# Performance work log

Measured on AMD Instinct MI355X. Metric: run time of the kernel, lower is better.

## Reference

```python
import jax, jax.numpy as jnp
import numpy as np

C = 256
DK = C // 8  # query/key channels


def setup_inputs() -> dict:
    key = jax.random.key(0)
    ks = jax.random.split(key, 7)
    B, W, H = 4, 64, 64
    x = jax.random.normal(ks[0], (B, C, W, H), dtype=jnp.float32)
    s_in = 1.0 / np.sqrt(C)
    Wq = jax.random.normal(ks[1], (DK, C), dtype=jnp.float32) * s_in
    bq = jnp.zeros((DK,), dtype=jnp.float32)
    Wk = jax.random.normal(ks[2], (DK, C), dtype=jnp.float32) * s_in
    bk = jnp.zeros((DK,), dtype=jnp.float32)
    Wv = jax.random.normal(ks[3], (C, C), dtype=jnp.float32) * s_in
    bv = jnp.zeros((C,), dtype=jnp.float32)
    return {"x": x, "Wq": Wq, "bq": bq, "Wk": Wk, "bk": bk, "Wv": Wv, "bv": bv}


def reference(x, Wq, bq, Wk, bk, Wv, bv):
    B, Cc, W, H = x.shape
    N = W * H
    xf = x.reshape(B, Cc, N)  # (B, C, N) flattened spatial
    # 1x1 convs == channel matmuls
    q = jnp.einsum('dc,bcn->bnd', Wq, xf) + bq  # (B, N, DK)
    k = jnp.einsum('dc,bcn->bdn', Wk, xf) + bk[None, :, None]  # (B, DK, N)
    v = jnp.einsum('oc,bcn->bon', Wv, xf) + bv[None, :, None]  # (B, C, N)
    energy = jnp.einsum('bnd,bdm->bnm', q, k) / jnp.sqrt(jnp.float32(q.shape[-1]))
    attn = jax.nn.softmax(energy, axis=-1)  # (B, N, N)
    out = jnp.einsum('bcn,bmn->bcm', v, attn)  # v @ attn^T
    return out.reshape(B, Cc, W, H) + x
```

## Files before the change

kernel.cpp:

```cpp
#include <hip/hip_runtime.h>
#include <hip/hip_bf16.h>
#include <math.h>

#define BB 4
#define CC 256
#define DKK 32
#define NN 4096
#define QSCALE 0.17677669529663687f

typedef __attribute__((ext_vector_type(8))) __bf16 bf16x8;
typedef __attribute__((ext_vector_type(4))) __bf16 bf16x4;
typedef __attribute__((ext_vector_type(4))) float f32x4;

__global__ __launch_bounds__(256) void prep_kernel(
    const float* __restrict__ x, __bf16* __restrict__ xT,
    const float* __restrict__ Wq, const float* __restrict__ Wk,
    const float* __restrict__ Wv, __bf16* __restrict__ Wb)
{
    __shared__ float xs[64][68];
    const int tid = threadIdx.x;
    const int n0 = blockIdx.x * 64;
    const int c0 = blockIdx.y * 64;
    const int b  = blockIdx.z;

    if (b == 0) {
        int unit = blockIdx.y * 64 + blockIdx.x;
        if (unit < 80) {
            int i = (unit * 256 + tid) * 4;
            int row = i >> 8, col = i & 255;
            const float* src;
            if (row < 32)      src = &Wq[row * 256 + col];
            else if (row < 64) src = &Wk[(row - 32) * 256 + col];
            else               src = &Wv[(row - 64) * 256 + col];
            float4 v = *(const float4*)src;
            Wb[i]     = (__bf16)v.x;
            Wb[i + 1] = (__bf16)v.y;
            Wb[i + 2] = (__bf16)v.z;
            Wb[i + 3] = (__bf16)v.w;
        }
    }

#pragma unroll
    for (int p = 0; p < 4; p++) {
        int cc = p * 16 + (tid >> 4);
        int nf = (tid & 15) * 4;
        float4 v = *(const float4*)&x[((size_t)(b * CC + c0 + cc)) * NN + n0 + nf];
        xs[cc][nf] = v.x; xs[cc][nf + 1] = v.y; xs[cc][nf + 2] = v.z; xs[cc][nf + 3] = v.w;
    }
    __syncthreads();
    int n = tid >> 2, cs = (tid & 3) * 16;
    bf16x8 lo, hi;
#pragma unroll
    for (int j = 0; j < 8; j++) {
        lo[j] = (__bf16)xs[cs + j][n];
        hi[j] = (__bf16)xs[cs + 8 + j][n];
    }
    size_t base = ((size_t)(b * NN + n0 + n)) * CC + c0 + cs;
    *(bf16x8*)&xT[base]     = lo;
    *(bf16x8*)&xT[base + 8] = hi;
}

__global__ __launch_bounds__(256) void qkv_kernel(
    const __bf16* __restrict__ xT, const __bf16* __restrict__ Wb,
    const float* __restrict__ bq, const float* __restrict__ bk,
    const float* __restrict__ bv,
    __bf16* __restrict__ qws, __bf16* __restrict__ kws, __bf16* __restrict__ vws)
{
    __shared__ float scr[64][33];

    const int tid = threadIdx.x;
    const int w   = tid >> 6;
    const int l   = tid & 63;
    const int l15 = l & 15;
    const int lq  = l >> 4;
    const int n0  = blockIdx.x * 32;
    const int b   = blockIdx.y;

    const __bf16* xbase = xT + ((size_t)b * NN + n0 + l15) * CC + lq * 8;
    const __bf16* wbase = Wb + (size_t)(80 * w + l15) * CC + lq * 8;

    const f32x4 zf = {0.f, 0.f, 0.f, 0.f};
    f32x4 acc[5][2];
#pragma unroll
    for (int i = 0; i < 5; i++)
#pragma unroll
        for (int j = 0; j < 2; j++) acc[i][j] = zf;

    bf16x8 bcur[2], acur[5], bnxt[2], anxt[5];
#pragma unroll
    for (int nt = 0; nt < 2; nt++) bcur[nt] = *(const bf16x8*)(xbase + nt * 16 * CC);
#pragma unroll
    for (int ot = 0; ot < 5; ot++) acur[ot] = *(const bf16x8*)(wbase + ot * 16 * CC);

#pragma unroll
    for (int ks = 0; ks < 8; ks++) {
        if (ks < 7) {
#pragma unroll
            for (int nt = 0; nt < 2; nt++)
                bnxt[nt] = *(const bf16x8*)(xbase + nt * 16 * CC + (ks + 1) * 32);
#pragma unroll
            for (int ot = 0; ot < 5; ot++)
                anxt[ot] = *(const bf16x8*)(wbase + ot * 16 * CC + (ks + 1) * 32);
        }
#pragma unroll
        for (int ot = 0; ot < 5; ot++)
#pragma unroll
            for (int nt = 0; nt < 2; nt++)
                acc[ot][nt] = __builtin_amdgcn_mfma_f32_16x16x32_bf16(acur[ot], bcur[nt], acc[ot][nt], 0, 0, 0);
        if (ks < 7) {
#pragma unroll
            for (int nt = 0; nt < 2; nt++) bcur[nt] = bnxt[nt];
#pragma unroll
            for (int ot = 0; ot < 5; ot++) acur[ot] = anxt[ot];
        }
    }

    __bf16* vchunk = vws + (size_t)b * CC * NN + (size_t)(n0 >> 5) * 16 * 512;
#pragma unroll
    for (int ot = 0; ot < 5; ot++) {
        int ob = 80 * w + ot * 16;
#pragma unroll
        for (int nt = 0; nt < 2; nt++) {
#pragma unroll
            for (int r = 0; r < 4; r++) {
                int o = ob + lq * 4 + r;
                int n = nt * 16 + l15;
                float val = acc[ot][nt][r];
                if (ob >= 64) {
                    int c = o - 64;
                    vchunk[(5 * w - 4 + ot) * 512 + (lq * 4 + r) * 32 + n] =
                        (__bf16)(val + bv[c]);
                } else if (ob < 32) {
                    scr[o][n] = (val + bq[o]) * QSCALE;
                } else {
                    scr[o][n] = val + bk[o - 32];
                }
            }
        }
    }
    __syncthreads();
    {
        int n  = tid >> 3;
        int d0 = (tid & 7) * 4;
        bf16x4 qv, kv;
#pragma unroll
        for (int j = 0; j < 4; j++) {
            qv[j] = (__bf16)scr[d0 + j][n];
            kv[j] = (__bf16)scr[32 + d0 + j][n];
        }
        size_t base = ((size_t)b * NN + n0 + n) * DKK + d0;
        *(bf16x4*)&qws[base] = qv;
        *(bf16x4*)&kws[base] = kv;
    }
}

#define PST 40
#define MST 68
#define PWSZ (64 * PST)

__global__ __launch_bounds__(256, 2) void attn_kernel(
    const __bf16* __restrict__ qb, const __bf16* __restrict__ kb,
    const __bf16* __restrict__ vt, const float* __restrict__ x,
    float* __restrict__ out)
{
    __shared__ __align__(16) unsigned char smem[42240];
    __bf16* pw   = (__bf16*)smem + (threadIdx.x >> 6) * 2 * PWSZ;
    float*  Ls   = (float*)(smem + 40960);
    float*  Linv = (float*)(smem + 41984);

    const int tid = threadIdx.x;
    const int w   = tid >> 6;
    const int l   = tid & 63;
    const int l15 = l & 15;
    const int lq  = l >> 4;

    const int beta = blockIdx.x;
    const int b    = (beta >> 1) & 3;
    const int ch   = (beta >> 3) & 1;
    const int mt   = ((beta >> 4) << 1) | (beta & 1);
    const int m0   = mt * 64;

    const __bf16* qbb = qb + (size_t)b * NN * DKK;
    const __bf16* kbb = kb + (size_t)b * NN * DKK;
    const __bf16* vtb = vt + (size_t)b * CC * NN;

    bf16x8 qa[4];
#pragma unroll
    for (int af = 0; af < 4; af++)
        qa[af] = *(const bf16x8*)(qbb + (size_t)(m0 + af * 16 + l15) * DKK + lq * 8);

    const __bf16* kstrip = kbb + (size_t)(w * 32 + l15) * DKK + lq * 8;
    const __bf16* vstrip = vtb + (size_t)w * 8192 + (size_t)ch * 4096
                               + l15 * 32 + lq * 8;

    const f32x4 zf = {0.f, 0.f, 0.f, 0.f};
    f32x4 acc[4][8];
#pragma unroll
    for (int i = 0; i < 4; i++)
#pragma unroll
        for (int j = 0; j < 8; j++) acc[i][j] = zf;
    float lacc[4] = {0.f, 0.f, 0.f, 0.f};

    bf16x8 kA0 = *(const bf16x8*)kstrip;
    bf16x8 kA1 = *(const bf16x8*)(kstrip + 16 * DKK);
#pragma unroll
    for (int af = 0; af < 4; af++) {
        f32x4 e0 = __builtin_amdgcn_mfma_f32_16x16x32_bf16(kA0, qa[af], zf, 0, 0, 0);
        f32x4 e1 = __builtin_amdgcn_mfma_f32_16x16x32_bf16(kA1, qa[af], zf, 0, 0, 0);
        bf16x4 p0, p1;
#pragma unroll
        for (int r = 0; r < 4; r++) {
            float v0 = __expf(e0[r]); lacc[af] += v0; p0[r] = (__bf16)v0;
            float v1 = __expf(e1[r]); lacc[af] += v1; p1[r] = (__bf16)v1;
        }
        *(bf16x4*)&pw[(af * 16 + l15) * PST + lq * 4]      = p0;
        *(bf16x4*)&pw[(af * 16 + l15) * PST + 16 + lq * 4] = p1;
    }
    kA0 = *(const bf16x8*)(kstrip + (size_t)128 * DKK);
    kA1 = *(const bf16x8*)(kstrip + (size_t)144 * DKK);

#pragma unroll 2
    for (int ic = 0; ic < 31; ic++) {
        const int cur = ic & 1;
        const __bf16* vch = vstrip + (size_t)ic * 32768;

        bf16x8 vfC[4], vfN[4];
#pragma unroll
        for (int ct = 0; ct < 4; ct++)
            vfC[ct] = *(const bf16x8*)(vch + ct * 512);

        bf16x8 pf[4];
#pragma unroll
        for (int af = 0; af < 4; af++)
            pf[af] = *(const bf16x8*)&pw[cur * PWSZ + (af * 16 + l15) * PST + lq * 8];

#pragma unroll
        for (int af = 0; af < 4; af++) {
            f32x4 e0 = __builtin_amdgcn_mfma_f32_16x16x32_bf16(kA0, qa[af], zf, 0, 0, 0);
            f32x4 e1 = __builtin_amdgcn_mfma_f32_16x16x32_bf16(kA1, qa[af], zf, 0, 0, 0);
            bf16x4 p0, p1;
#pragma unroll
            for (int r = 0; r < 4; r++) {
                float v0 = __expf(e0[r]); lacc[af] += v0; p0[r] = (__bf16)v0;
                float v1 = __expf(e1[r]); lacc[af] += v1; p1[r] = (__bf16)v1;
            }
            *(bf16x4*)&pw[(cur ^ 1) * PWSZ + (af * 16 + l15) * PST + lq * 4]      = p0;
            *(bf16x4*)&pw[(cur ^ 1) * PWSZ + (af * 16 + l15) * PST + 16 + lq * 4] = p1;
        }
        kA0 = *(const bf16x8*)(kstrip + (size_t)(ic + 2) * 128 * DKK);
        kA1 = *(const bf16x8*)(kstrip + (size_t)((ic + 2) * 128 + 16) * DKK);

#pragma unroll
        for (int ct = 0; ct < 4; ct++)
            vfN[ct] = *(const bf16x8*)(vch + (4 + ct) * 512);
#pragma unroll
        for (int ct = 0; ct < 4; ct++)
#pragma unroll
            for (int af = 0; af < 4; af++)
                acc[af][ct] = __builtin_amdgcn_mfma_f32_16x16x32_bf16(vfC[ct], pf[af], acc[af][ct], 0, 0, 0);
#pragma unroll
        for (int ct = 0; ct < 4; ct++)
#pragma unroll
            for (int af = 0; af < 4; af++)
                acc[af][4 + ct] = __builtin_amdgcn_mfma_f32_16x16x32_bf16(vfN[ct], pf[af], acc[af][4 + ct], 0, 0, 0);
    }

    {
        const __bf16* vch = vstrip + (size_t)31 * 32768;
        bf16x8 pf[4];
#pragma unroll
        for (int af = 0; af < 4; af++)
            pf[af] = *(const bf16x8*)&pw[(31 & 1) * PWSZ + (af * 16 + l15) * PST + lq * 8];
        bf16x8 vfC[4], vfN[4];
#pragma unroll
        for (int ct = 0; ct < 4; ct++) vfC[ct] = *(const bf16x8*)(vch + ct * 512);
#pragma unroll
        for (int ct = 0; ct < 4; ct++) vfN[ct] = *(const bf16x8*)(vch + (4 + ct) * 512);
#pragma unroll
        for (int ct = 0; ct < 4; ct++)
#pragma unroll
            for (int af = 0; af < 4; af++)
                acc[af][ct] = __builtin_amdgcn_mfma_f32_16x16x32_bf16(vfC[ct], pf[af], acc[af][ct], 0, 0, 0);
#pragma unroll
        for (int ct = 0; ct < 4; ct++)
#pragma unroll
            for (int af = 0; af < 4; af++)
                acc[af][4 + ct] = __builtin_amdgcn_mfma_f32_16x16x32_bf16(vfN[ct], pf[af], acc[af][4 + ct], 0, 0, 0);
    }

#pragma unroll
    for (int af = 0; af < 4; af++) {
        lacc[af] += __shfl_xor(lacc[af], 16, 64);
        lacc[af] += __shfl_xor(lacc[af], 32, 64);
    }
    if (lq == 0) {
#pragma unroll
        for (int af = 0; af < 4; af++) Ls[w * 64 + af * 16 + l15] = lacc[af];
    }
    __syncthreads();
    if (tid < 64)
        Linv[tid] = 1.0f / (Ls[tid] + Ls[64 + tid] + Ls[128 + tid] + Ls[192 + tid]);

    float* Ored = (float*)smem + w * (32 * MST);
#pragma unroll
    for (int q = 0; q < 4; q++) {
        if (q > 0) __syncthreads();
#pragma unroll
        for (int ctp = 0; ctp < 2; ctp++) {
            int ct = 2 * q + ctp;
#pragma unroll
            for (int af = 0; af < 4; af++) {
#pragma unroll
                for (int r = 0; r < 4; r++)
                    Ored[(ctp * 16 + lq * 4 + r) * MST + af * 16 + l15] = acc[af][ct][r];
            }
        }
        __syncthreads();
        const int cl  = tid >> 3;
        const int mi0 = (tid & 7) * 8;
        const float* Ob = (const float*)smem + cl * MST;
#pragma unroll
        for (int j = 0; j < 2; j++) {
            int mi = mi0 + 4 * j;
            f32x4 s = *(const f32x4*)&Ob[mi];
            s = s + *(const f32x4*)&Ob[1 * (32 * MST) + mi];
            s = s + *(const f32x4*)&Ob[2 * (32 * MST) + mi];
            s = s + *(const f32x4*)&Ob[3 * (32 * MST) + mi];
            f32x4 li = *(const f32x4*)&Linv[mi];
            int c = ch * 128 + q * 32 + cl;
            size_t gi = ((size_t)(b * CC + c)) * NN + m0 + mi;
            f32x4 xr = *(const f32x4*)&x[gi];
            *(f32x4*)&out[gi] = s * li + xr;
        }
    }
}

extern "C" void kernel_launch(void* const* d_in, const int* in_sizes, int n_in,
                              void* d_out, int out_size, void* d_ws, size_t ws_size,
                              hipStream_t stream) {
    const float* x  = (const float*)d_in[0];
    const float* Wq = (const float*)d_in[1];
    const float* bq = (const float*)d_in[2];
    const float* Wk = (const float*)d_in[3];
    const float* bk = (const float*)d_in[4];
    const float* Wv = (const float*)d_in[5];
    const float* bv = (const float*)d_in[6];
    float* out = (float*)d_out;

    __bf16* qws = (__bf16*)d_ws;
    __bf16* kws = qws + (size_t)BB * NN * DKK;
    __bf16* vws = kws + (size_t)BB * NN * DKK;
    __bf16* Wb  = vws + (size_t)BB * CC * NN;
    __bf16* xT  = Wb  + (size_t)320 * CC;

    prep_kernel<<<dim3(64, 4, BB), 256, 0, stream>>>(x, xT, Wq, Wk, Wv, Wb);
    qkv_kernel <<<dim3(128, BB), 256, 0, stream>>>(xT, Wb, bq, bk, bv, qws, kws, vws);
    attn_kernel<<<dim3(512), 256, 0, stream>>>(qws, kws, vws, x, out);
}
```

Measured before the change: 152.3 us.

## Fuse input transpose and weight conversion into QKV kernel; use exp2 softmax

```diff
diff --git a/kernel.cpp b/kernel.cpp
--- a/kernel.cpp
+++ b/kernel.cpp
@@ -6,121 +6,125 @@
 #define CC 256
 #define DKK 32
 #define NN 4096
-#define QSCALE 0.17677669529663687f
+#define QSCALE 0.2550181864060454f
 
 typedef __attribute__((ext_vector_type(8))) __bf16 bf16x8;
 typedef __attribute__((ext_vector_type(4))) __bf16 bf16x4;
 typedef __attribute__((ext_vector_type(4))) float f32x4;
 
-__global__ __launch_bounds__(256) void prep_kernel(
-    const float* __restrict__ x, __bf16* __restrict__ xT,
-    const float* __restrict__ Wq, const float* __restrict__ Wk,
-    const float* __restrict__ Wv, __bf16* __restrict__ Wb)
-{
-    __shared__ float xs[64][68];
-    const int tid = threadIdx.x;
-    const int n0 = blockIdx.x * 64;
-    const int c0 = blockIdx.y * 64;
-    const int b  = blockIdx.z;
-
-    if (b == 0) {
-        int unit = blockIdx.y * 64 + blockIdx.x;
-        if (unit < 80) {
-            int i = (unit * 256 + tid) * 4;
-            int row = i >> 8, col = i & 255;
-            const float* src;
-            if (row < 32)      src = &Wq[row * 256 + col];
-            else if (row < 64) src = &Wk[(row - 32) * 256 + col];
-            else               src = &Wv[(row - 64) * 256 + col];
-            float4 v = *(const float4*)src;
-            Wb[i]     = (__bf16)v.x;
-            Wb[i + 1] = (__bf16)v.y;
-            Wb[i + 2] = (__bf16)v.z;
-            Wb[i + 3] = (__bf16)v.w;
-        }
-    }
-
-#pragma unroll
-    for (int p = 0; p < 4; p++) {
-        int cc = p * 16 + (tid >> 4);
-        int nf = (tid & 15) * 4;
-        float4 v = *(const float4*)&x[((size_t)(b * CC + c0 + cc)) * NN + n0 + nf];
-        xs[cc][nf] = v.x; xs[cc][nf + 1] = v.y; xs[cc][nf + 2] = v.z; xs[cc][nf + 3] = v.w;
-    }
-    __syncthreads();
-    int n = tid >> 2, cs = (tid & 3) * 16;
-    bf16x8 lo, hi;
-#pragma unroll
-    for (int j = 0; j < 8; j++) {
-        lo[j] = (__bf16)xs[cs + j][n];
-        hi[j] = (__bf16)xs[cs + 8 + j][n];
-    }
-    size_t base = ((size_t)(b * NN + n0 + n)) * CC + c0 + cs;
-    *(bf16x8*)&xT[base]     = lo;
-    *(bf16x8*)&xT[base + 8] = hi;
-}
+#define XST 260
+#define SCRST 65
 
 __global__ __launch_bounds__(256) void qkv_kernel(
-    const __bf16* __restrict__ xT, const __bf16* __restrict__ Wb,
-    const float* __restrict__ bq, const float* __restrict__ bk,
-    const float* __restrict__ bv,
+    const float* __restrict__ x,
+    const float* __restrict__ Wq, const float* __restrict__ bq,
+    const float* __restrict__ Wk, const float* __restrict__ bk,
+    const float* __restrict__ Wv, const float* __restrict__ bv,
     __bf16* __restrict__ qws, __bf16* __restrict__ kws, __bf16* __restrict__ vws)
 {
-    __shared__ float scr[64][33];
+    __shared__ __align__(16) unsigned char smem[50688];
+    __bf16* xsT  = (__bf16*)smem;
+    float*  xs32 = (float*)(smem + 33280);
+    float*  scr  = (float*)(smem + 33280);
 
     const int tid = threadIdx.x;
     const int w   = tid >> 6;
     const int l   = tid & 63;
     const int l15 = l & 15;
     const int lq  = l >> 4;
-    const int n0  = blockIdx.x * 32;
+    const int n0  = blockIdx.x * 64;
     const int b   = blockIdx.y;
 
-    const __bf16* xbase = xT + ((size_t)b * NN + n0 + l15) * CC + lq * 8;
-    const __bf16* wbase = Wb + (size_t)(80 * w + l15) * CC + lq * 8;
+    for (int cr = 0; cr < 4; cr++) {
+#pragma unroll
+        for (int p = 0; p < 4; p++) {
+            int cc = p * 16 + (tid >> 4);
+            int nf = (tid & 15) * 4;
+            float4 v = *(const float4*)&x[((size_t)(b * CC + cr * 64 + cc)) * NN + n0 + nf];
+            *(float4*)&xs32[cc * 68 + nf] = v;
+        }
+        __syncthreads();
+        {
+            int n = tid >> 2, cs = (tid & 3) * 16;
+            bf16x4 t0, t1, t2, t3;
+#pragma unroll
+            for (int j = 0; j < 4; j++) {
+                t0[j] = (__bf16)xs32[(cs + j)      * 68 + n];
+                t1[j] = (__bf16)xs32[(cs + 4 + j)  * 68 + n];
+                t2[j] = (__bf16)xs32[(cs + 8 + j)  * 68 + n];
+                t3[j] = (__bf16)xs32[(cs + 12 + j) * 68 + n];
+            }
+            *(bf16x4*)&xsT[n * XST + cr * 64 + cs]      = t0;
+            *(bf16x4*)&xsT[n * XST + cr * 64 + cs + 4]  = t1;
+            *(bf16x4*)&xsT[n * XST + cr * 64 + cs + 8]  = t2;
+            *(bf16x4*)&xsT[n * XST + cr * 64 + cs + 12] = t3;
+        }
+        __syncthreads();
+    }
+
+    const float* wp[5];
+#pragma unroll
+    for (int ot = 0; ot < 5; ot++) {
+        int ob = 80 * w + 16 * ot;
+        const float* src = (ob < 32) ? (Wq + (size_t)ob * CC)
+                         : (ob < 64) ? (Wk + (size_t)(ob - 32) * CC)
+                                     : (Wv + (size_t)(ob - 64) * CC);
+        wp[ot] = src + (size_t)l15 * CC;
+    }
 
     const f32x4 zf = {0.f, 0.f, 0.f, 0.f};
-    f32x4 acc[5][2];
+    f32x4 acc[5][4];
 #pragma unroll
     for (int i = 0; i < 5; i++)
 #pragma unroll
-        for (int j = 0; j < 2; j++) acc[i][j] = zf;
-
-    bf16x8 bcur[2], acur[5], bnxt[2], anxt[5];
-#pragma unroll
-    for (int nt = 0; nt < 2; nt++) bcur[nt] = *(const bf16x8*)(xbase + nt * 16 * CC);
-#pragma unroll
-    for (int ot = 0; ot < 5; ot++) acur[ot] = *(const bf16x8*)(wbase + ot * 16 * CC);
-
+        for (int j = 0; j < 4; j++) acc[i][j] = zf;
+
+    float4 wc[5][2], wn[5][2];
+#pragma unroll
+    for (int ot = 0; ot < 5; ot++) {
+        wc[ot][0] = *(const float4*)(wp[ot] + lq * 8);
+        wc[ot][1] = *(const float4*)(wp[ot] + lq * 8 + 4);
+    }
 #pragma unroll
     for (int ks = 0; ks < 8; ks++) {
         if (ks < 7) {
 #pragma unroll
-            for (int nt = 0; nt < 2; nt++)
-                bnxt[nt] = *(const bf16x8*)(xbase + nt * 16 * CC + (ks + 1) * 32);
-#pragma unroll
-            for (int ot = 0; ot < 5; ot++)
-                anxt[ot] = *(const bf16x8*)(wbase + ot * 16 * CC + (ks + 1) * 32);
-        }
-#pragma unroll
-        for (int ot = 0; ot < 5; ot++)
-#pragma unroll
-            for (int nt = 0; nt < 2; nt++)
-                acc[ot][nt] = __builtin_amdgcn_mfma_f32_16x16x32_bf16(acur[ot], bcur[nt], acc[ot][nt], 0, 0, 0);
+            for (int ot = 0; ot < 5; ot++) {
+                wn[ot][0] = *(const float4*)(wp[ot] + (ks + 1) * 32 + lq * 8);
+                wn[ot][1] = *(const float4*)(wp[ot] + (ks + 1) * 32 + lq * 8 + 4);
+            }
+        }
+        bf16x8 bfr[4];
+#pragma unroll
+        for (int nt = 0; nt < 4; nt++) {
+            bf16x4 lo = *(const bf16x4*)&xsT[(nt * 16 + l15) * XST + ks * 32 + lq * 8];
+            bf16x4 hi = *(const bf16x4*)&xsT[(nt * 16 + l15) * XST + ks * 32 + lq * 8 + 4];
+            bfr[nt] = __builtin_shufflevector(lo, hi, 0, 1, 2, 3, 4, 5, 6, 7);
+        }
+#pragma unroll
+        for (int ot = 0; ot < 5; ot++) {
+            bf16x8 af;
+            af[0] = (__bf16)wc[ot][0].x; af[1] = (__bf16)wc[ot][0].y;
+            af[2] = (__bf16)wc[ot][0].z; af[3] = (__bf16)wc[ot][0].w;
+            af[4] = (__bf16)wc[ot][1].x; af[5] = (__bf16)wc[ot][1].y;
+            af[6] = (__bf16)wc[ot][1].z; af[7] = (__bf16)wc[ot][1].w;
+#pragma unroll
+            for (int nt = 0; nt < 4; nt++)
+                acc[ot][nt] = __builtin_amdgcn_mfma_f32_16x16x32_bf16(af, bfr[nt], acc[ot][nt], 0, 0, 0);
+        }
         if (ks < 7) {
 #pragma unroll
-            for (int nt = 0; nt < 2; nt++) bcur[nt] = bnxt[nt];
-#pragma unroll
-            for (int ot = 0; ot < 5; ot++) acur[ot] = anxt[ot];
-        }
-    }
-
-    __bf16* vchunk = vws + (size_t)b * CC * NN + (size_t)(n0 >> 5) * 16 * 512;
+            for (int ot = 0; ot < 5; ot++) { wc[ot][0] = wn[ot][0]; wc[ot][1] = wn[ot][1]; }
+        }
+    }
+
+    __syncthreads();
+    const size_t vbase = (size_t)b * CC * NN;
 #pragma unroll
     for (int ot = 0; ot < 5; ot++) {
         int ob = 80 * w + ot * 16;
 #pragma unroll
-        for (int nt = 0; nt < 2; nt++) {
+        for (int nt = 0; nt < 4; nt++) {
 #pragma unroll
             for (int r = 0; r < 4; r++) {
                 int o = ob + lq * 4 + r;
@@ -128,33 +132,34 @@
                 float val = acc[ot][nt][r];
                 if (ob >= 64) {
                     int c = o - 64;
-                    vchunk[(5 * w - 4 + ot) * 512 + (lq * 4 + r) * 32 + n] =
-                        (__bf16)(val + bv[c]);
+                    int chunk = (n0 >> 5) + (nt >> 1);
+                    vws[vbase + (size_t)chunk * 8192 + (5 * w - 4 + ot) * 512
+                        + (lq * 4 + r) * 32 + (nt & 1) * 16 + l15] = (__bf16)(val + bv[c]);
                 } else if (ob < 32) {
-                    scr[o][n] = (val + bq[o]) * QSCALE;
+                    scr[o * SCRST + n] = (val + bq[o]) * QSCALE;
                 } else {
-                    scr[o][n] = val + bk[o - 32];
+                    scr[o * SCRST + n] = val + bk[o - 32];
                 }
             }
         }
     }
     __syncthreads();
     {
-        int n  = tid >> 3;
-        int d0 = (tid & 7) * 4;
-        bf16x4 qv, kv;
-#pragma unroll
-        for (int j = 0; j < 4; j++) {
-            qv[j] = (__bf16)scr[d0 + j][n];
-            kv[j] = (__bf16)scr[32 + d0 + j][n];
+        int n  = tid >> 2;
+        int d0 = (tid & 3) * 8;
+        bf16x8 qv, kv;
+#pragma unroll
+        for (int j = 0; j < 8; j++) {
+            qv[j] = (__bf16)scr[(d0 + j) * SCRST + n];
+            kv[j] = (__bf16)scr[(32 + d0 + j) * SCRST + n];
         }
         size_t base = ((size_t)b * NN + n0 + n) * DKK + d0;
-        *(bf16x4*)&qws[base] = qv;
-        *(bf16x4*)&kws[base] = kv;
+        *(bf16x8*)&qws[base] = qv;
+        *(bf16x8*)&kws[base] = kv;
     }
 }
 
-#define PST 40
+#define PST 36
 #define MST 68
 #define PWSZ (64 * PST)
 
@@ -163,10 +168,10 @@
     const __bf16* __restrict__ vt, const float* __restrict__ x,
     float* __restrict__ out)
 {
-    __shared__ __align__(16) unsigned char smem[42240];
+    __shared__ __align__(16) unsigned char smem[38144];
     __bf16* pw   = (__bf16*)smem + (threadIdx.x >> 6) * 2 * PWSZ;
-    float*  Ls   = (float*)(smem + 40960);
-    float*  Linv = (float*)(smem + 41984);
+    float*  Ls   = (float*)(smem + 36864);
+    float*  Linv = (float*)(smem + 37888);
 
     const int tid = threadIdx.x;
     const int w   = tid >> 6;
@@ -210,8 +215,8 @@
         bf16x4 p0, p1;
 #pragma unroll
         for (int r = 0; r < 4; r++) {
-            float v0 = __expf(e0[r]); lacc[af] += v0; p0[r] = (__bf16)v0;
-            float v1 = __expf(e1[r]); lacc[af] += v1; p1[r] = (__bf16)v1;
+            float v0 = __builtin_amdgcn_exp2f(e0[r]); lacc[af] += v0; p0[r] = (__bf16)v0;
+            float v1 = __builtin_amdgcn_exp2f(e1[r]); lacc[af] += v1; p1[r] = (__bf16)v1;
         }
         *(bf16x4*)&pw[(af * 16 + l15) * PST + lq * 4]      = p0;
         *(bf16x4*)&pw[(af * 16 + l15) * PST + 16 + lq * 4] = p1;
@@ -231,8 +236,11 @@
 
         bf16x8 pf[4];
 #pragma unroll
-        for (int af = 0; af < 4; af++)
-            pf[af] = *(const bf16x8*)&pw[cur * PWSZ + (af * 16 + l15) * PST + lq * 8];
+        for (int af = 0; af < 4; af++) {
+            bf16x4 plo = *(const bf16x4*)&pw[cur * PWSZ + (af * 16 + l15) * PST + lq * 8];
+            bf16x4 phi = *(const bf16x4*)&pw[cur * PWSZ + (af * 16 + l15) * PST + lq * 8 + 4];
+            pf[af] = __builtin_shufflevector(plo, phi, 0, 1, 2, 3, 4, 5, 6, 7);
+        }
 
 #pragma unroll
         for (int af = 0; af < 4; af++) {
@@ -241,8 +249,8 @@
             bf16x4 p0, p1;
 #pragma unroll
             for (int r = 0; r < 4; r++) {
-                float v0 = __expf(e0[r]); lacc[af] += v0; p0[r] = (__bf16)v0;
-                float v1 = __expf(e1[r]); lacc[af] += v1; p1[r] = (__bf16)v1;
+                float v0 = __builtin_amdgcn_exp2f(e0[r]); lacc[af] += v0; p0[r] = (__bf16)v0;
+                float v1 = __builtin_amdgcn_exp2f(e1[r]); lacc[af] += v1; p1[r] = (__bf16)v1;
             }
             *(bf16x4*)&pw[(cur ^ 1) * PWSZ + (af * 16 + l15) * PST + lq * 4]      = p0;
             *(bf16x4*)&pw[(cur ^ 1) * PWSZ + (af * 16 + l15) * PST + 16 + lq * 4] = p1;
@@ -269,8 +277,11 @@
         const __bf16* vch = vstrip + (size_t)31 * 32768;
         bf16x8 pf[4];
 #pragma unroll
-        for (int af = 0; af < 4; af++)
-            pf[af] = *(const bf16x8*)&pw[(31 & 1) * PWSZ + (af * 16 + l15) * PST + lq * 8];
+        for (int af = 0; af < 4; af++) {
+            bf16x4 plo = *(const bf16x4*)&pw[(31 & 1) * PWSZ + (af * 16 + l15) * PST + lq * 8];
+            bf16x4 phi = *(const bf16x4*)&pw[(31 & 1) * PWSZ + (af * 16 + l15) * PST + lq * 8 + 4];
+            pf[af] = __builtin_shufflevector(plo, phi, 0, 1, 2, 3, 4, 5, 6, 7);
+        }
         bf16x8 vfC[4], vfN[4];
 #pragma unroll
         for (int ct = 0; ct < 4; ct++) vfC[ct] = *(const bf16x8*)(vch + ct * 512);
@@ -350,10 +361,8 @@
     __bf16* qws = (__bf16*)d_ws;
     __bf16* kws = qws + (size_t)BB * NN * DKK;
     __bf16* vws = kws + (size_t)BB * NN * DKK;
-    __bf16* Wb  = vws + (size_t)BB * CC * NN;
-    __bf16* xT  = Wb  + (size_t)320 * CC;
-
-    prep_kernel<<<dim3(64, 4, BB), 256, 0, stream>>>(x, xT, Wq, Wk, Wv, Wb);
-    qkv_kernel <<<dim3(128, BB), 256, 0, stream>>>(xT, Wb, bq, bk, bv, qws, kws, vws);
+
+    qkv_kernel<<<dim3(64, BB), 256, 0, stream>>>(x, Wq, bq, Wk, bk, Wv, bv,
+                                                 qws, kws, vws);
     attn_kernel<<<dim3(512), 256, 0, stream>>>(qws, kws, vws, x, out);
 }
```

After: 157.4 us. 3.3% more time.
